# Performance work log

Measured on AMD Instinct MI355X. Metric: run time of the kernel, lower is better.

The kernel has to match this reference:

```python
import jax, jax.numpy as jnp
import numpy as np

N = 100000
E = 3200000
D = 512

def setup_inputs() -> dict:
    key = jax.random.key(0)
    ks = jax.random.split(key, 6)
    X = jax.random.normal(ks[0], (N, D), dtype=jnp.float32)
    edge_row = jax.random.randint(ks[1], (E,), 0, N, dtype=jnp.int32)
    edge_col = jax.random.randint(ks[2], (E,), 0, N, dtype=jnp.int32)
    edge_val = jax.random.uniform(ks[3], (E,), dtype=jnp.float32)
    # glorot-uniform-ish init for weights
    lim = (6.0 / (D + D)) ** 0.5
    W1 = jax.random.uniform(ks[4], (D, D), dtype=jnp.float32, minval=-lim, maxval=lim)
    W2 = jax.random.uniform(ks[5], (D, D), dtype=jnp.float32, minval=-lim, maxval=lim)
    return {"X": X, "edge_row": edge_row, "edge_col": edge_col,
            "edge_val": edge_val, "W1": W1, "W2": W2}

def _spmm(edge_row, edge_col, edge_val, H):
    # out[r] = sum_{e: row[e]==r} val[e] * H[col[e]]
    msgs = edge_val[:, None] * H[edge_col]          # [E, D]
    return jax.ops.segment_sum(msgs, edge_row, num_segments=N)

def reference(X, edge_row, edge_col, edge_val, W1, W2):
    # layer 1: An @ (X @ W1), tanh activation, no bias
    h = jnp.tanh(_spmm(edge_row, edge_col, edge_val, X @ W1))
    # layer 2
    h = jnp.tanh(_spmm(edge_row, edge_col, edge_val, h @ W2))
    # tf.nn.l2_normalize(curr, axis=1)
    norm = jnp.sqrt(jnp.maximum(jnp.sum(h * h, axis=1, keepdims=True), 1e-12))
    return h / norm
```

## Files before the change

kernel.cpp:

```cpp
#include <hip/hip_runtime.h>
#include <hip/hip_fp16.h>

#define D_DIM 512

typedef __attribute__((ext_vector_type(8))) _Float16 half8;
typedef __attribute__((ext_vector_type(4))) float f32x4;
typedef __attribute__((ext_vector_type(2))) float float2v;

__device__ inline unsigned short f16b(float f) {
  return __half_as_ushort(__float2half(f));
}


__device__ inline void glds16(const _Float16* g, _Float16* l) {
  __builtin_amdgcn_global_load_lds(
      (const __attribute__((address_space(1))) void*)g,
      (__attribute__((address_space(3))) void*)l, 16, 0, 0);
}


__global__ __launch_bounds__(1024) void k_scanA(const int* __restrict__ cnt, int* __restrict__ rp,
                                                int* __restrict__ bsum, int n) {
  __shared__ int s[1024];
  int i = blockIdx.x * 1024 + threadIdx.x;
  int v = (i < n) ? cnt[i] : 0;
  s[threadIdx.x] = v;
  __syncthreads();
  for (int off = 1; off < 1024; off <<= 1) {
    int t = (threadIdx.x >= off) ? s[threadIdx.x - off] : 0;
    __syncthreads();
    s[threadIdx.x] += t;
    __syncthreads();
  }
  if (i < n) rp[i] = s[threadIdx.x] - v;
  if (threadIdx.x == 1023) bsum[blockIdx.x] = s[1023];
}

__global__ __launch_bounds__(1024) void k_scanB(int* __restrict__ bsum, int nb) {
  __shared__ int s[1024];
  int v = (threadIdx.x < nb) ? bsum[threadIdx.x] : 0;
  s[threadIdx.x] = v;
  __syncthreads();
  for (int off = 1; off < 1024; off <<= 1) {
    int t = (threadIdx.x >= off) ? s[threadIdx.x - off] : 0;
    __syncthreads();
    s[threadIdx.x] += t;
    __syncthreads();
  }
  if (threadIdx.x < nb) bsum[threadIdx.x] = s[threadIdx.x] - v;
}

__global__ __launch_bounds__(256) void k_scanC(int* __restrict__ rp, const int* __restrict__ bsum, int n, int E) {
  int i = blockIdx.x * 256 + threadIdx.x;
  if (i < n) rp[i] += bsum[i >> 10];
  if (i == 0) rp[n] = E;
}


__global__ __launch_bounds__(256) void k_fusedA(const float* __restrict__ X, unsigned* __restrict__ Xf, int N,
                                                const int* __restrict__ erow, int* __restrict__ cnt,
                                                int* __restrict__ rank, int E,
                                                const float* __restrict__ W1, _Float16* __restrict__ W1f,
                                                const float* __restrict__ W2, _Float16* __restrict__ W2f,
                                                int C ) {
  __shared__ unsigned lds[4096];
  const int id = blockIdx.x;
  const int tid = threadIdx.x;
  if (id < 3 * C) {
    const int rem = id % 3;
    if (rem == 0) {
      const int Rg = id / 3;
      const long r0 = (long)Rg * 16;
#pragma unroll
      for (int k = 0; k < 8; ++k) {
        int idx = tid + k * 256;
        int r = idx >> 7;
        int q = idx & 127;
        int c0 = q * 4;
        float4 x = make_float4(0.f, 0.f, 0.f, 0.f);
        long gr = r0 + r;
        if (gr < N) x = ((const float4*)X)[gr * 128 + q];
        unsigned h0 = (unsigned)f16b(x.x) | ((unsigned)f16b(x.y) << 16);
        unsigned h1 = (unsigned)f16b(x.z) | ((unsigned)f16b(x.w) << 16);
        int off = (c0 >> 5) * 512 + ((c0 >> 3) & 3) * 128 + r * 8 + (c0 & 7);
        lds[off >> 1] = h0;
        lds[(off >> 1) + 1] = h1;
      }
      __syncthreads();
      uint4* dst = (uint4*)(Xf + (long)Rg * 4096);
      const uint4* src = (const uint4*)lds;
#pragma unroll
      for (int k = 0; k < 4; ++k) dst[tid + k * 256] = src[tid + k * 256];
    } else {
      const int hi = (id / 3) * 2 + rem - 1;
      const int i = hi * 256 + tid;
      if (i < E) {
        int k = atomicAdd(&cnt[erow[i]], 1);
        rank[i] = k;
      }
    }
  } else {
    const int rb = id - 3 * C;
    const float* W = (rb < 128) ? W1 : W2;
    _Float16* Wf = (rb < 128) ? W1f : W2f;
    const int rb2 = rb & 127;
    const int kg = rb2 >> 1;
    const int n = (rb2 & 1) * 256 + tid;
    half8 v;
#pragma unroll
    for (int j = 0; j < 8; ++j) v[j] = (_Float16)W[(kg * 8 + j) * D_DIM + n];
    const long halfidx = ((long)(kg >> 2) * 32 + (n >> 4)) * 512 + (kg & 3) * 128 + (n & 15) * 8;
    *(half8*)(Wf + halfidx) = v;
  }
}


__global__ __launch_bounds__(256) void k_fusedB(const _Float16* __restrict__ A,
                                                const _Float16* __restrict__ B,
                                                _Float16* __restrict__ Cout, int MB,
                                                const int* __restrict__ row, const int* __restrict__ col,
                                                const float* __restrict__ val, const int* __restrict__ rp,
                                                const int* __restrict__ rank,
                                                int2* __restrict__ edat, int E) {
  __shared__ __align__(16) char smem[32768];
  const int id = blockIdx.x;
  const int tid = threadIdx.x;

  if (id % 5 != 0) {
    const int si = (id / 5) * 4 + (id % 5) - 1;
    const int i = si * 256 + tid;
    if (i < E) {
      int r = row[i];
      int p = rp[r] + rank[i];
      edat[p] = make_int2(col[i], __float_as_int(val[i]));
    }
    return;
  }

  const int gi = id / 5;
  const int sgrid = gi >> 3;
  const int vxcd = (5 * gi) & 7;
  const int panel = (sgrid >> 2) * 8 + vxcd;
  if (panel >= MB) return;
  const int nb = sgrid & 3;

  const int lane = tid & 63;
  const int w = tid >> 6;
  const int wr = w >> 1, wc = w & 1;
  const int c = lane & 15, g = lane >> 4;
  const long r0 = (long)panel * 128 + wr * 64;
  const int n0 = nb * 128 + wc * 64;

  _Float16* Asl = (_Float16*)smem;
  _Float16* Bsl = (_Float16*)(smem + 16384);

  f32x4 acc[4][4] = {};

  const int f0 = w, f1 = w + 4;
  const long aF0 = ((long)(panel * 8 + f0) * 16) * 512 + lane * 8;
  const long aF1 = ((long)(panel * 8 + f1) * 16) * 512 + lane * 8;
  const long bBase = ((long)nb * 8) * 512 + lane * 8;

  for (int s = 0; s < 8; ++s) {
    const int k5a = 2 * s, k5b = 2 * s + 1;
    glds16(A + aF0 + (long)k5a * 512, Asl + (0 * 8 + f0) * 512);
    glds16(A + aF0 + (long)k5b * 512, Asl + (1 * 8 + f0) * 512);
    glds16(A + aF1 + (long)k5a * 512, Asl + (0 * 8 + f1) * 512);
    glds16(A + aF1 + (long)k5b * 512, Asl + (1 * 8 + f1) * 512);
    glds16(B + bBase + ((long)k5a * 32 + f0) * 512, Bsl + (0 * 8 + f0) * 512);
    glds16(B + bBase + ((long)k5b * 32 + f0) * 512, Bsl + (1 * 8 + f0) * 512);
    glds16(B + bBase + ((long)k5a * 32 + f1) * 512, Bsl + (0 * 8 + f1) * 512);
    glds16(B + bBase + ((long)k5b * 32 + f1) * 512, Bsl + (1 * 8 + f1) * 512);
    __syncthreads();
#pragma unroll
    for (int k5loc = 0; k5loc < 2; ++k5loc) {
      half8 a[4], b[4];
#pragma unroll
      for (int mi = 0; mi < 4; ++mi)
        a[mi] = *(const half8*)(Asl + (k5loc * 8 + wr * 4 + mi) * 512 + lane * 8);
#pragma unroll
      for (int ni = 0; ni < 4; ++ni)
        b[ni] = *(const half8*)(Bsl + (k5loc * 8 + wc * 4 + ni) * 512 + lane * 8);
#pragma unroll
      for (int mi = 0; mi < 4; ++mi)
#pragma unroll
        for (int ni = 0; ni < 4; ++ni)
          acc[mi][ni] = __builtin_amdgcn_mfma_f32_16x16x32_f16(a[mi], b[ni], acc[mi][ni], 0, 0, 0);
    }
    __syncthreads();
  }

  float (*ep)[16][68] = (float (*)[16][68])smem;
#pragma unroll
  for (int m = 0; m < 4; ++m) {
#pragma unroll
    for (int nf = 0; nf < 4; ++nf)
#pragma unroll
      for (int j = 0; j < 4; ++j)
        ep[w][g * 4 + j][nf * 16 + c] = acc[m][nf][j];
    __syncthreads();
    {
      const int rw = lane >> 2;
      const int ch = lane & 3;
      float v[16];
#pragma unroll
      for (int q = 0; q < 16; ++q) v[q] = ep[w][rw][ch * 16 + q];
      half8 h0, h1;
#pragma unroll
      for (int q = 0; q < 8; ++q) {
        h0[q] = (_Float16)v[q];
        h1[q] = (_Float16)v[8 + q];
      }
      _Float16* dst = Cout + (r0 + m * 16 + rw) * D_DIM + n0 + ch * 16;
      *(half8*)dst = h0;
      *(half8*)(dst + 8) = h1;
    }
    __syncthreads();
  }
}


__global__ __launch_bounds__(256) void k_gemm(const _Float16* __restrict__ A,
                                              const _Float16* __restrict__ B,
                                              _Float16* __restrict__ Cout, int MB) {
  const int id = blockIdx.x;
  const int xcd = id & 7;
  const int sgrid = id >> 3;
  const int panel = (sgrid >> 2) * 8 + xcd;
  if (panel >= MB) return;
  const int nb = sgrid & 3;

  const int tid = threadIdx.x;
  const int lane = tid & 63;
  const int w = tid >> 6;
  const int wr = w >> 1, wc = w & 1;
  const int c = lane & 15, g = lane >> 4;
  const long r0 = (long)panel * 128 + wr * 64;
  const int n0 = nb * 128 + wc * 64;

  __shared__ __align__(16) char smem[32768];
  _Float16* Asl = (_Float16*)smem;
  _Float16* Bsl = (_Float16*)(smem + 16384);

  f32x4 acc[4][4] = {};

  const int f0 = w, f1 = w + 4;
  const long aF0 = ((long)(panel * 8 + f0) * 16) * 512 + lane * 8;
  const long aF1 = ((long)(panel * 8 + f1) * 16) * 512 + lane * 8;
  const long bBase = ((long)nb * 8) * 512 + lane * 8;

  for (int s = 0; s < 8; ++s) {
    const int k5a = 2 * s, k5b = 2 * s + 1;
    glds16(A + aF0 + (long)k5a * 512, Asl + (0 * 8 + f0) * 512);
    glds16(A + aF0 + (long)k5b * 512, Asl + (1 * 8 + f0) * 512);
    glds16(A + aF1 + (long)k5a * 512, Asl + (0 * 8 + f1) * 512);
    glds16(A + aF1 + (long)k5b * 512, Asl + (1 * 8 + f1) * 512);
    glds16(B + bBase + ((long)k5a * 32 + f0) * 512, Bsl + (0 * 8 + f0) * 512);
    glds16(B + bBase + ((long)k5b * 32 + f0) * 512, Bsl + (1 * 8 + f0) * 512);
    glds16(B + bBase + ((long)k5a * 32 + f1) * 512, Bsl + (0 * 8 + f1) * 512);
    glds16(B + bBase + ((long)k5b * 32 + f1) * 512, Bsl + (1 * 8 + f1) * 512);
    __syncthreads();
#pragma unroll
    for (int k5loc = 0; k5loc < 2; ++k5loc) {
      half8 a[4], b[4];
#pragma unroll
      for (int mi = 0; mi < 4; ++mi)
        a[mi] = *(const half8*)(Asl + (k5loc * 8 + wr * 4 + mi) * 512 + lane * 8);
#pragma unroll
      for (int ni = 0; ni < 4; ++ni)
        b[ni] = *(const half8*)(Bsl + (k5loc * 8 + wc * 4 + ni) * 512 + lane * 8);
#pragma unroll
      for (int mi = 0; mi < 4; ++mi)
#pragma unroll
        for (int ni = 0; ni < 4; ++ni)
          acc[mi][ni] = __builtin_amdgcn_mfma_f32_16x16x32_f16(a[mi], b[ni], acc[mi][ni], 0, 0, 0);
    }
    __syncthreads();
  }

  float (*ep)[16][68] = (float (*)[16][68])smem;
#pragma unroll
  for (int m = 0; m < 4; ++m) {
#pragma unroll
    for (int nf = 0; nf < 4; ++nf)
#pragma unroll
      for (int j = 0; j < 4; ++j)
        ep[w][g * 4 + j][nf * 16 + c] = acc[m][nf][j];
    __syncthreads();
    {
      const int rw = lane >> 2;
      const int ch = lane & 3;
      float v[16];
#pragma unroll
      for (int q = 0; q < 16; ++q) v[q] = ep[w][rw][ch * 16 + q];
      half8 h0, h1;
#pragma unroll
      for (int q = 0; q < 8; ++q) {
        h0[q] = (_Float16)v[q];
        h1[q] = (_Float16)v[8 + q];
      }
      _Float16* dst = Cout + (r0 + m * 16 + rw) * D_DIM + n0 + ch * 16;
      *(half8*)dst = h0;
      *(half8*)(dst + 8) = h1;
    }
    __syncthreads();
  }
}


template <int MODE>
__global__ __launch_bounds__(256) void k_spmm(const unsigned short* __restrict__ T, const int* __restrict__ rp,
                                              const int2* __restrict__ edat,
                                              unsigned* __restrict__ Hf, float* __restrict__ out) {
  __shared__ float p[4][D_DIM];
  __shared__ float wss[4];
  const int r = blockIdx.x;
  const int tid = threadIdx.x;
  const int w = tid >> 6, lane = tid & 63;
  const int beg = rp[r], end = rp[r + 1];
  const int cnt = end - beg;
  const int eb = beg + ((cnt * w) >> 2);
  const int ee = beg + ((cnt * (w + 1)) >> 2);

  float acc[8] = {};
  const uint4* Tv = (const uint4*)T;
  for (int e = eb; e < ee; ++e) {
    const int2 ed = edat[e];
    const float v = __int_as_float(ed.y);
    uint4 x = Tv[(long)ed.x * 64 + lane];
    unsigned xs[4] = {x.x, x.y, x.z, x.w};
#pragma unroll
    for (int q = 0; q < 4; ++q) {
      float2 f = __half22float2(__builtin_bit_cast(__half2, xs[q]));
      acc[2 * q] = fmaf(v, f.x, acc[2 * q]);
      acc[2 * q + 1] = fmaf(v, f.y, acc[2 * q + 1]);
    }
  }
  *(float4*)&p[w][lane * 8] = make_float4(acc[0], acc[1], acc[2], acc[3]);
  *(float4*)&p[w][lane * 8 + 4] = make_float4(acc[4], acc[5], acc[6], acc[7]);
  __syncthreads();

  const int c = tid * 2;
  float s0 = p[0][c] + p[1][c] + p[2][c] + p[3][c];
  float s1 = p[0][c + 1] + p[1][c + 1] + p[2][c + 1] + p[3][c + 1];
  s0 = tanhf(s0);
  s1 = tanhf(s1);

  if (MODE == 0) {
    unsigned hv = (unsigned)f16b(s0) | ((unsigned)f16b(s1) << 16);
    const long halfidx = ((long)(r >> 4) * 16 + (c >> 5)) * 512 + ((c >> 3) & 3) * 128 + (r & 15) * 8 + (c & 7);
    __builtin_nontemporal_store(hv, Hf + (halfidx >> 1));
  } else {
    float ss = fmaf(s0, s0, s1 * s1);
#pragma unroll
    for (int off = 1; off < 64; off <<= 1) ss += __shfl_xor(ss, off);
    if (lane == 0) wss[w] = ss;
    __syncthreads();
    const float tot = wss[0] + wss[1] + wss[2] + wss[3];
    const float sc = rsqrtf(fmaxf(tot, 1e-12f));
    float2v o;
    o.x = s0 * sc;
    o.y = s1 * sc;
    __builtin_nontemporal_store(o, (float2v*)out + (long)r * 256 + tid);
  }
}


extern "C" void kernel_launch(void* const* d_in, const int* in_sizes, int n_in,
                              void* d_out, int out_size, void* d_ws, size_t ws_size,
                              hipStream_t stream) {
  const float* X = (const float*)d_in[0];
  const int* erow = (const int*)d_in[1];
  const int* ecol = (const int*)d_in[2];
  const float* evalv = (const float*)d_in[3];
  const float* W1 = (const float*)d_in[4];
  const float* W2 = (const float*)d_in[5];
  const int N = in_sizes[0] / D_DIM;
  const int E = in_sizes[1];
  (void)n_in; (void)out_size; (void)ws_size;

  const int MB = (N + 127) / 128;
  const long Mp = (long)MB * 128;

  char* wsp = (char*)d_ws;
  size_t off = 0;
  auto alloc = [&](size_t bytes) {
    void* p = wsp + off;
    off = (off + bytes + 255) & ~(size_t)255;
    return p;
  };
  unsigned short* T  = (unsigned short*)alloc(Mp * D_DIM * 2);
  unsigned* Af = (unsigned*)alloc(Mp * D_DIM * 2);
  int2* edat  = (int2*)alloc((size_t)E * 8);
  int* rankArr = (int*)alloc((size_t)E * 4);
  int* rowptr = (int*)alloc((size_t)(N + 1) * 4);
  int* cnt    = (int*)alloc((size_t)N * 4);
  int* bsum   = (int*)alloc(1024 * 4);
  _Float16* W1f = (_Float16*)alloc((size_t)D_DIM * D_DIM * 2);
  _Float16* W2f = (_Float16*)alloc((size_t)D_DIM * D_DIM * 2);

  const int nScanBlk = (N + 1023) / 1024;
  const int gemmGrid = 32 * ((MB + 7) / 8);
  const int convBlocks = (int)(Mp / 16);

  hipMemsetAsync(cnt, 0, (size_t)N * 4, stream);
  k_fusedA<<<dim3(3 * convBlocks + 256), dim3(256), 0, stream>>>(
      X, Af, N, erow, cnt, rankArr, E, W1, W1f, W2, W2f, convBlocks);

  k_scanA<<<dim3(nScanBlk), dim3(1024), 0, stream>>>(cnt, rowptr, bsum, N);
  k_scanB<<<dim3(1), dim3(1024), 0, stream>>>(bsum, nScanBlk);
  k_scanC<<<dim3((N + 255) / 256), dim3(256), 0, stream>>>(rowptr, bsum, N, E);

  k_fusedB<<<dim3(5 * gemmGrid), dim3(256), 0, stream>>>(
      (const _Float16*)Af, W1f, (_Float16*)T, MB, erow, ecol, evalv, rowptr, rankArr, edat, E);

  k_spmm<0><<<dim3(N), dim3(256), 0, stream>>>(T, rowptr, edat, Af, nullptr);
  k_gemm<<<dim3(gemmGrid), dim3(256), 0, stream>>>((const _Float16*)Af, W2f, (_Float16*)T, MB);
  k_spmm<1><<<dim3(N), dim3(256), 0, stream>>>(T, rowptr, edat, nullptr, (float*)d_out);
}
```

Baseline: 1.320 ms.

## Overlap layer-2 GEMM with tail of layer-1 SpMM via row split

Splits the layer-1 aggregation at a panel-aligned row boundary. The GEMM panels that only depend on already-aggregated rows run in a fused launch alongside the remaining SpMM rows. The GEMM output goes to a separate workspace buffer T2 so it does not clobber T, which is still being read. The goal is to hide the GEMM compute behind the memory-bound gather and remove a serialization point. It costs extra workspace and falls back to the old sequence if that workspace is unavailable.

```diff
diff --git a/kernel.cpp b/kernel.cpp
--- a/kernel.cpp
+++ b/kernel.cpp
@@ -62,7 +62,7 @@
                                                 int* __restrict__ rank, int E,
                                                 const float* __restrict__ W1, _Float16* __restrict__ W1f,
                                                 const float* __restrict__ W2, _Float16* __restrict__ W2f,
-                                                int C ) {
+                                                int C) {
   __shared__ unsigned lds[4096];
   const int id = blockIdx.x;
   const int tid = threadIdx.x;
@@ -115,6 +115,140 @@
 }
 
 
+__device__ inline void gemm_body(const _Float16* __restrict__ A, const _Float16* __restrict__ B,
+                                 _Float16* __restrict__ Cout, int panel, int nb, int tid, char* smem) {
+  const int lane = tid & 63;
+  const int w = tid >> 6;
+  const int wr = w >> 1, wc = w & 1;
+  const int c = lane & 15, g = lane >> 4;
+  const long r0 = (long)panel * 128 + wr * 64;
+  const int n0 = nb * 128 + wc * 64;
+
+  _Float16* Asl = (_Float16*)smem;
+  _Float16* Bsl = (_Float16*)(smem + 16384);
+
+  f32x4 acc[4][4] = {};
+
+  const int f0 = w, f1 = w + 4;
+  const long aF0 = ((long)(panel * 8 + f0) * 16) * 512 + lane * 8;
+  const long aF1 = ((long)(panel * 8 + f1) * 16) * 512 + lane * 8;
+  const long bBase = ((long)nb * 8) * 512 + lane * 8;
+
+  for (int s = 0; s < 8; ++s) {
+    const int k5a = 2 * s, k5b = 2 * s + 1;
+    glds16(A + aF0 + (long)k5a * 512, Asl + (0 * 8 + f0) * 512);
+    glds16(A + aF0 + (long)k5b * 512, Asl + (1 * 8 + f0) * 512);
+    glds16(A + aF1 + (long)k5a * 512, Asl + (0 * 8 + f1) * 512);
+    glds16(A + aF1 + (long)k5b * 512, Asl + (1 * 8 + f1) * 512);
+    glds16(B + bBase + ((long)k5a * 32 + f0) * 512, Bsl + (0 * 8 + f0) * 512);
+    glds16(B + bBase + ((long)k5b * 32 + f0) * 512, Bsl + (1 * 8 + f0) * 512);
+    glds16(B + bBase + ((long)k5a * 32 + f1) * 512, Bsl + (0 * 8 + f1) * 512);
+    glds16(B + bBase + ((long)k5b * 32 + f1) * 512, Bsl + (1 * 8 + f1) * 512);
+    __syncthreads();
+#pragma unroll
+    for (int k5loc = 0; k5loc < 2; ++k5loc) {
+      half8 a[4], b[4];
+#pragma unroll
+      for (int mi = 0; mi < 4; ++mi)
+        a[mi] = *(const half8*)(Asl + (k5loc * 8 + wr * 4 + mi) * 512 + lane * 8);
+#pragma unroll
+      for (int ni = 0; ni < 4; ++ni)
+        b[ni] = *(const half8*)(Bsl + (k5loc * 8 + wc * 4 + ni) * 512 + lane * 8);
+#pragma unroll
+      for (int mi = 0; mi < 4; ++mi)
+#pragma unroll
+        for (int ni = 0; ni < 4; ++ni)
+          acc[mi][ni] = __builtin_amdgcn_mfma_f32_16x16x32_f16(a[mi], b[ni], acc[mi][ni], 0, 0, 0);
+    }
+    __syncthreads();
+  }
+
+  float (*ep)[16][68] = (float (*)[16][68])smem;
+#pragma unroll
+  for (int m = 0; m < 4; ++m) {
+#pragma unroll
+    for (int nf = 0; nf < 4; ++nf)
+#pragma unroll
+      for (int j = 0; j < 4; ++j)
+        ep[w][g * 4 + j][nf * 16 + c] = acc[m][nf][j];
+    __syncthreads();
+    {
+      const int rw = lane >> 2;
+      const int ch = lane & 3;
+      float v[16];
+#pragma unroll
+      for (int q = 0; q < 16; ++q) v[q] = ep[w][rw][ch * 16 + q];
+      half8 h0, h1;
+#pragma unroll
+      for (int q = 0; q < 8; ++q) {
+        h0[q] = (_Float16)v[q];
+        h1[q] = (_Float16)v[8 + q];
+      }
+      _Float16* dst = Cout + (r0 + m * 16 + rw) * D_DIM + n0 + ch * 16;
+      *(half8*)dst = h0;
+      *(half8*)(dst + 8) = h1;
+    }
+    __syncthreads();
+  }
+}
+
+
+template <int MODE>
+__device__ inline void spmm_body(const unsigned short* __restrict__ T, const int* __restrict__ rp,
+                                 const int2* __restrict__ edat, unsigned* __restrict__ Hf,
+                                 float* __restrict__ out, int r, int tid, char* smem) {
+  float (*p)[D_DIM] = (float (*)[D_DIM])smem;
+  float* wss = (float*)(smem + 4 * D_DIM * 4);
+  const int w = tid >> 6, lane = tid & 63;
+  const int beg = rp[r], end = rp[r + 1];
+  const int cnt = end - beg;
+  const int eb = beg + ((cnt * w) >> 2);
+  const int ee = beg + ((cnt * (w + 1)) >> 2);
+
+  float acc[8] = {};
+  const uint4* Tv = (const uint4*)T;
+  for (int e = eb; e < ee; ++e) {
+    const int2 ed = edat[e];
+    const float v = __int_as_float(ed.y);
+    uint4 x = Tv[(long)ed.x * 64 + lane];
+    unsigned xs[4] = {x.x, x.y, x.z, x.w};
+#pragma unroll
+    for (int q = 0; q < 4; ++q) {
+      float2 f = __half22float2(__builtin_bit_cast(__half2, xs[q]));
+      acc[2 * q] = fmaf(v, f.x, acc[2 * q]);
+      acc[2 * q + 1] = fmaf(v, f.y, acc[2 * q + 1]);
+    }
+  }
+  *(float4*)&p[w][lane * 8] = make_float4(acc[0], acc[1], acc[2], acc[3]);
+  *(float4*)&p[w][lane * 8 + 4] = make_float4(acc[4], acc[5], acc[6], acc[7]);
+  __syncthreads();
+
+  const int c = tid * 2;
+  float s0 = p[0][c] + p[1][c] + p[2][c] + p[3][c];
+  float s1 = p[0][c + 1] + p[1][c + 1] + p[2][c + 1] + p[3][c + 1];
+  s0 = tanhf(s0);
+  s1 = tanhf(s1);
+
+  if (MODE == 0) {
+    unsigned hv = (unsigned)f16b(s0) | ((unsigned)f16b(s1) << 16);
+    const long halfidx = ((long)(r >> 4) * 16 + (c >> 5)) * 512 + ((c >> 3) & 3) * 128 + (r & 15) * 8 + (c & 7);
+    __builtin_nontemporal_store(hv, Hf + (halfidx >> 1));
+  } else {
+    float ss = fmaf(s0, s0, s1 * s1);
+#pragma unroll
+    for (int off = 1; off < 64; off <<= 1) ss += __shfl_xor(ss, off);
+    if (lane == 0) wss[w] = ss;
+    __syncthreads();
+    const float tot = wss[0] + wss[1] + wss[2] + wss[3];
+    const float sc = rsqrtf(fmaxf(tot, 1e-12f));
+    float2v o;
+    o.x = s0 * sc;
+    o.y = s1 * sc;
+    __builtin_nontemporal_store(o, (float2v*)out + (long)r * 256 + tid);
+  }
+}
+
+
 __global__ __launch_bounds__(256) void k_fusedB(const _Float16* __restrict__ A,
                                                 const _Float16* __restrict__ B,
                                                 _Float16* __restrict__ Cout, int MB,
@@ -131,238 +265,61 @@
     const int i = si * 256 + tid;
     if (i < E) {
       int r = row[i];
-      int p = rp[r] + rank[i];
-      edat[p] = make_int2(col[i], __float_as_int(val[i]));
+      edat[rp[r] + rank[i]] = make_int2(col[i], __float_as_int(val[i]));
     }
     return;
   }
-
   const int gi = id / 5;
   const int sgrid = gi >> 3;
   const int vxcd = (5 * gi) & 7;
   const int panel = (sgrid >> 2) * 8 + vxcd;
   if (panel >= MB) return;
-  const int nb = sgrid & 3;
-
-  const int lane = tid & 63;
-  const int w = tid >> 6;
-  const int wr = w >> 1, wc = w & 1;
-  const int c = lane & 15, g = lane >> 4;
-  const long r0 = (long)panel * 128 + wr * 64;
-  const int n0 = nb * 128 + wc * 64;
-
-  _Float16* Asl = (_Float16*)smem;
-  _Float16* Bsl = (_Float16*)(smem + 16384);
-
-  f32x4 acc[4][4] = {};
-
-  const int f0 = w, f1 = w + 4;
-  const long aF0 = ((long)(panel * 8 + f0) * 16) * 512 + lane * 8;
-  const long aF1 = ((long)(panel * 8 + f1) * 16) * 512 + lane * 8;
-  const long bBase = ((long)nb * 8) * 512 + lane * 8;
-
-  for (int s = 0; s < 8; ++s) {
-    const int k5a = 2 * s, k5b = 2 * s + 1;
-    glds16(A + aF0 + (long)k5a * 512, Asl + (0 * 8 + f0) * 512);
-    glds16(A + aF0 + (long)k5b * 512, Asl + (1 * 8 + f0) * 512);
-    glds16(A + aF1 + (long)k5a * 512, Asl + (0 * 8 + f1) * 512);
-    glds16(A + aF1 + (long)k5b * 512, Asl + (1 * 8 + f1) * 512);
-    glds16(B + bBase + ((long)k5a * 32 + f0) * 512, Bsl + (0 * 8 + f0) * 512);
-    glds16(B + bBase + ((long)k5b * 32 + f0) * 512, Bsl + (1 * 8 + f0) * 512);
-    glds16(B + bBase + ((long)k5a * 32 + f1) * 512, Bsl + (0 * 8 + f1) * 512);
-    glds16(B + bBase + ((long)k5b * 32 + f1) * 512, Bsl + (1 * 8 + f1) * 512);
-    __syncthreads();
-#pragma unroll
-    for (int k5loc = 0; k5loc < 2; ++k5loc) {
-      half8 a[4], b[4];
-#pragma unroll
-      for (int mi = 0; mi < 4; ++mi)
-        a[mi] = *(const half8*)(Asl + (k5loc * 8 + wr * 4 + mi) * 512 + lane * 8);
-#pragma unroll
-      for (int ni = 0; ni < 4; ++ni)
-        b[ni] = *(const half8*)(Bsl + (k5loc * 8 + wc * 4 + ni) * 512 + lane * 8);
-#pragma unroll
-      for (int mi = 0; mi < 4; ++mi)
-#pragma unroll
-        for (int ni = 0; ni < 4; ++ni)
-          acc[mi][ni] = __builtin_amdgcn_mfma_f32_16x16x32_f16(a[mi], b[ni], acc[mi][ni], 0, 0, 0);
-    }
-    __syncthreads();
-  }
-
-  float (*ep)[16][68] = (float (*)[16][68])smem;
-#pragma unroll
-  for (int m = 0; m < 4; ++m) {
-#pragma unroll
-    for (int nf = 0; nf < 4; ++nf)
-#pragma unroll
-      for (int j = 0; j < 4; ++j)
-        ep[w][g * 4 + j][nf * 16 + c] = acc[m][nf][j];
-    __syncthreads();
-    {
-      const int rw = lane >> 2;
-      const int ch = lane & 3;
-      float v[16];
-#pragma unroll
-      for (int q = 0; q < 16; ++q) v[q] = ep[w][rw][ch * 16 + q];
-      half8 h0, h1;
-#pragma unroll
-      for (int q = 0; q < 8; ++q) {
-        h0[q] = (_Float16)v[q];
-        h1[q] = (_Float16)v[8 + q];
-      }
-      _Float16* dst = Cout + (r0 + m * 16 + rw) * D_DIM + n0 + ch * 16;
-      *(half8*)dst = h0;
-      *(half8*)(dst + 8) = h1;
-    }
-    __syncthreads();
+  gemm_body(A, B, Cout, panel, sgrid & 3, tid, smem);
+}
+
+
+__global__ __launch_bounds__(256) void k_fusedC(const unsigned short* __restrict__ T, const int* __restrict__ rp,
+                                                const int2* __restrict__ edat, unsigned* __restrict__ Hf,
+                                                const _Float16* __restrict__ A, const _Float16* __restrict__ B,
+                                                _Float16* __restrict__ T2, int panelEnd,
+                                                int rowOff, int rowCnt) {
+  __shared__ __align__(16) char smem[32768];
+  const int id = blockIdx.x;
+  const int tid = threadIdx.x;
+  const int g22 = id / 22, r22 = id % 22;
+  if (r22 == 0) {
+    const int gi = g22;
+    const int xcd = gi & 7;
+    const int sgrid = gi >> 3;
+    const int panel = (sgrid >> 2) * 8 + xcd;
+    if (panel >= panelEnd) return;
+    gemm_body(A, B, T2, panel, sgrid & 3, tid, smem);
+  } else {
+    const int si = g22 * 21 + r22 - 1;
+    if (si >= rowCnt) return;
+    spmm_body<0>(T, rp, edat, Hf, nullptr, rowOff + si, tid, smem);
   }
 }
 
 
 __global__ __launch_bounds__(256) void k_gemm(const _Float16* __restrict__ A,
                                               const _Float16* __restrict__ B,
-                                              _Float16* __restrict__ Cout, int MB) {
+                                              _Float16* __restrict__ Cout, int panel0, int panelEnd) {
+  __shared__ __align__(16) char smem[32768];
   const int id = blockIdx.x;
   const int xcd = id & 7;
   const int sgrid = id >> 3;
-  const int panel = (sgrid >> 2) * 8 + xcd;
-  if (panel >= MB) return;
-  const int nb = sgrid & 3;
-
-  const int tid = threadIdx.x;
-  const int lane = tid & 63;
-  const int w = tid >> 6;
-  const int wr = w >> 1, wc = w & 1;
-  const int c = lane & 15, g = lane >> 4;
-  const long r0 = (long)panel * 128 + wr * 64;
-  const int n0 = nb * 128 + wc * 64;
-
-  __shared__ __align__(16) char smem[32768];
-  _Float16* Asl = (_Float16*)smem;
-  _Float16* Bsl = (_Float16*)(smem + 16384);
-
-  f32x4 acc[4][4] = {};
-
-  const int f0 = w, f1 = w + 4;
-  const long aF0 = ((long)(panel * 8 + f0) * 16) * 512 + lane * 8;
-  const long aF1 = ((long)(panel * 8 + f1) * 16) * 512 + lane * 8;
-  const long bBase = ((long)nb * 8) * 512 + lane * 8;
-
-  for (int s = 0; s < 8; ++s) {
-    const int k5a = 2 * s, k5b = 2 * s + 1;
-    glds16(A + aF0 + (long)k5a * 512, Asl + (0 * 8 + f0) * 512);
-    glds16(A + aF0 + (long)k5b * 512, Asl + (1 * 8 + f0) * 512);
-    glds16(A + aF1 + (long)k5a * 512, Asl + (0 * 8 + f1) * 512);
-    glds16(A + aF1 + (long)k5b * 512, Asl + (1 * 8 + f1) * 512);
-    glds16(B + bBase + ((long)k5a * 32 + f0) * 512, Bsl + (0 * 8 + f0) * 512);
-    glds16(B + bBase + ((long)k5b * 32 + f0) * 512, Bsl + (1 * 8 + f0) * 512);
-    glds16(B + bBase + ((long)k5a * 32 + f1) * 512, Bsl + (0 * 8 + f1) * 512);
-    glds16(B + bBase + ((long)k5b * 32 + f1) * 512, Bsl + (1 * 8 + f1) * 512);
-    __syncthreads();
-#pragma unroll
-    for (int k5loc = 0; k5loc < 2; ++k5loc) {
-      half8 a[4], b[4];
-#pragma unroll
-      for (int mi = 0; mi < 4; ++mi)
-        a[mi] = *(const half8*)(Asl + (k5loc * 8 + wr * 4 + mi) * 512 + lane * 8);
-#pragma unroll
-      for (int ni = 0; ni < 4; ++ni)
-        b[ni] = *(const half8*)(Bsl + (k5loc * 8 + wc * 4 + ni) * 512 + lane * 8);
-#pragma unroll
-      for (int mi = 0; mi < 4; ++mi)
-#pragma unroll
-        for (int ni = 0; ni < 4; ++ni)
-          acc[mi][ni] = __builtin_amdgcn_mfma_f32_16x16x32_f16(a[mi], b[ni], acc[mi][ni], 0, 0, 0);
-    }
-    __syncthreads();
-  }
-
-  float (*ep)[16][68] = (float (*)[16][68])smem;
-#pragma unroll
-  for (int m = 0; m < 4; ++m) {
-#pragma unroll
-    for (int nf = 0; nf < 4; ++nf)
-#pragma unroll
-      for (int j = 0; j < 4; ++j)
-        ep[w][g * 4 + j][nf * 16 + c] = acc[m][nf][j];
-    __syncthreads();
-    {
-      const int rw = lane >> 2;
-      const int ch = lane & 3;
-      float v[16];
-#pragma unroll
-      for (int q = 0; q < 16; ++q) v[q] = ep[w][rw][ch * 16 + q];
-      half8 h0, h1;
-#pragma unroll
-      for (int q = 0; q < 8; ++q) {
-        h0[q] = (_Float16)v[q];
-        h1[q] = (_Float16)v[8 + q];
-      }
-      _Float16* dst = Cout + (r0 + m * 16 + rw) * D_DIM + n0 + ch * 16;
-      *(half8*)dst = h0;
-      *(half8*)(dst + 8) = h1;
-    }
-    __syncthreads();
-  }
-}
-
+  const int panel = panel0 + (sgrid >> 2) * 8 + xcd;
+  if (panel >= panelEnd) return;
+  gemm_body(A, B, Cout, panel, sgrid & 3, threadIdx.x, smem);
+}
 
 template <int MODE>
 __global__ __launch_bounds__(256) void k_spmm(const unsigned short* __restrict__ T, const int* __restrict__ rp,
                                               const int2* __restrict__ edat,
-                                              unsigned* __restrict__ Hf, float* __restrict__ out) {
-  __shared__ float p[4][D_DIM];
-  __shared__ float wss[4];
-  const int r = blockIdx.x;
-  const int tid = threadIdx.x;
-  const int w = tid >> 6, lane = tid & 63;
-  const int beg = rp[r], end = rp[r + 1];
-  const int cnt = end - beg;
-  const int eb = beg + ((cnt * w) >> 2);
-  const int ee = beg + ((cnt * (w + 1)) >> 2);
-
-  float acc[8] = {};
-  const uint4* Tv = (const uint4*)T;
-  for (int e = eb; e < ee; ++e) {
-    const int2 ed = edat[e];
-    const float v = __int_as_float(ed.y);
-    uint4 x = Tv[(long)ed.x * 64 + lane];
-    unsigned xs[4] = {x.x, x.y, x.z, x.w};
-#pragma unroll
-    for (int q = 0; q < 4; ++q) {
-      float2 f = __half22float2(__builtin_bit_cast(__half2, xs[q]));
-      acc[2 * q] = fmaf(v, f.x, acc[2 * q]);
-      acc[2 * q + 1] = fmaf(v, f.y, acc[2 * q + 1]);
-    }
-  }
-  *(float4*)&p[w][lane * 8] = make_float4(acc[0], acc[1], acc[2], acc[3]);
-  *(float4*)&p[w][lane * 8 + 4] = make_float4(acc[4], acc[5], acc[6], acc[7]);
-  __syncthreads();
-
-  const int c = tid * 2;
-  float s0 = p[0][c] + p[1][c] + p[2][c] + p[3][c];
-  float s1 = p[0][c + 1] + p[1][c + 1] + p[2][c + 1] + p[3][c + 1];
-  s0 = tanhf(s0);
-  s1 = tanhf(s1);
-
-  if (MODE == 0) {
-    unsigned hv = (unsigned)f16b(s0) | ((unsigned)f16b(s1) << 16);
-    const long halfidx = ((long)(r >> 4) * 16 + (c >> 5)) * 512 + ((c >> 3) & 3) * 128 + (r & 15) * 8 + (c & 7);
-    __builtin_nontemporal_store(hv, Hf + (halfidx >> 1));
-  } else {
-    float ss = fmaf(s0, s0, s1 * s1);
-#pragma unroll
-    for (int off = 1; off < 64; off <<= 1) ss += __shfl_xor(ss, off);
-    if (lane == 0) wss[w] = ss;
-    __syncthreads();
-    const float tot = wss[0] + wss[1] + wss[2] + wss[3];
-    const float sc = rsqrtf(fmaxf(tot, 1e-12f));
-    float2v o;
-    o.x = s0 * sc;
-    o.y = s1 * sc;
-    __builtin_nontemporal_store(o, (float2v*)out + (long)r * 256 + tid);
-  }
+                                              unsigned* __restrict__ Hf, float* __restrict__ out, int rowOff) {
+  __shared__ __align__(16) char smem[4 * D_DIM * 4 + 64];
+  spmm_body<MODE>(T, rp, edat, Hf, out, blockIdx.x + rowOff, threadIdx.x, smem);
 }
 
 
@@ -377,7 +334,7 @@
   const float* W2 = (const float*)d_in[5];
   const int N = in_sizes[0] / D_DIM;
   const int E = in_sizes[1];
-  (void)n_in; (void)out_size; (void)ws_size;
+  (void)n_in; (void)out_size;
 
   const int MB = (N + 127) / 128;
   const long Mp = (long)MB * 128;
@@ -398,6 +355,9 @@
   int* bsum   = (int*)alloc(1024 * 4);
   _Float16* W1f = (_Float16*)alloc((size_t)D_DIM * D_DIM * 2);
   _Float16* W2f = (_Float16*)alloc((size_t)D_DIM * D_DIM * 2);
+  _Float16* T2 = (_Float16*)alloc(Mp * D_DIM * 2);
+  const bool pipelined = (off <= ws_size);
+  if (!pipelined) T2 = (_Float16*)T;
 
   const int nScanBlk = (N + 1023) / 1024;
   const int gemmGrid = 32 * ((MB + 7) / 8);
@@ -414,7 +374,22 @@
   k_fusedB<<<dim3(5 * gemmGrid), dim3(256), 0, stream>>>(
       (const _Float16*)Af, W1f, (_Float16*)T, MB, erow, ecol, evalv, rowptr, rankArr, edat, E);
 
-  k_spmm<0><<<dim3(N), dim3(256), 0, stream>>>(T, rowptr, edat, Af, nullptr);
-  k_gemm<<<dim3(gemmGrid), dim3(256), 0, stream>>>((const _Float16*)Af, W2f, (_Float16*)T, MB);
-  k_spmm<1><<<dim3(N), dim3(256), 0, stream>>>(T, rowptr, edat, nullptr, (float*)d_out);
-}
+  if (pipelined) {
+    const int splitRows = 60032;
+    const int splitPanels = 469;
+    k_spmm<0><<<dim3(splitRows), dim3(256), 0, stream>>>(T, rowptr, edat, Af, nullptr, 0);
+    const int s1Rows = N - splitRows;
+    const int grpCnt = (s1Rows + 20) / 21;
+    k_fusedC<<<dim3(grpCnt * 22), dim3(256), 0, stream>>>(
+        T, rowptr, edat, Af, (const _Float16*)Af, W2f, T2, splitPanels, splitRows, s1Rows);
+    const int g1Panels = MB - splitPanels;
+    k_gemm<<<dim3(32 * ((g1Panels + 7) / 8)), dim3(256), 0, stream>>>(
+        (const _Float16*)Af, W2f, T2, splitPanels, MB);
+    k_spmm<1><<<dim3(N), dim3(256), 0, stream>>>((const unsigned short*)T2, rowptr, edat, nullptr,
+                                                 (float*)d_out, 0);
+  } else {
+    k_spmm<0><<<dim3(N), dim3(256), 0, stream>>>(T, rowptr, edat, Af, nullptr, 0);
+    k_gemm<<<dim3(gemmGrid), dim3(256), 0, stream>>>((const _Float16*)Af, W2f, (_Float16*)T, 0, MB);
+    k_spmm<1><<<dim3(N), dim3(256), 0, stream>>>(T, rowptr, edat, nullptr, (float*)d_out, 0);
+  }
+}
```

Result: slower. 1.476 ms (+11.8%).
